# Kernel tuning notes

Hardware: AMD Instinct MI355X
Metric: run time of the kernel (lower is better)

Reference implementation:

```python
import jax, jax.numpy as jnp
import numpy as np

N, E, DIN, DOUT = 50000, 500000, 512, 20
HID = DIN // 4  # 128, from GAT_NET(dim_in, dim_in//4, dim_out)
NEG_SLOPE = 0.2  # PyG GATConv default


def _gat_conv(x, src, dst, Wl, Wr, att_l, att_r, bias, n):
    """PyG GATConv with heads=1: messages flow src -> dst (source_to_target)."""
    xl = x @ Wl.T            # [N, C_out] source-side transform
    xr = x @ Wr.T            # [N, C_out] target-side transform
    el = jnp.sum(xl * att_l, axis=-1)   # [N]
    er = jnp.sum(xr * att_r, axis=-1)   # [N]
    e = jax.nn.leaky_relu(el[src] + er[dst], NEG_SLOPE)  # [E]
    # numerically-stable softmax over incoming edges of each dst node
    emax = jax.ops.segment_max(e, dst, num_segments=n)
    emax = jnp.where(jnp.isfinite(emax), emax, 0.0)  # guard isolated nodes
    w = jnp.exp(e - emax[dst])
    denom = jax.ops.segment_sum(w, dst, num_segments=n)
    alpha = w / (denom[dst] + 1e-16)                     # [E]
    out = jax.ops.segment_sum(xl[src] * alpha[:, None], dst, num_segments=n)
    return out + bias


def setup_inputs() -> dict:
    key = jax.random.key(0)
    ks = jax.random.split(key, 12)
    x = jax.random.normal(ks[0], (N, DIN), dtype=jnp.float32)
    edge_index = jax.random.randint(ks[1], (2, E), 0, N, dtype=jnp.int64)
    # mil_score0: Linear(dim_in, dim_out), init normal(std=0.01), bias 0
    W0 = 0.01 * jax.random.normal(ks[2], (DOUT, DIN), dtype=jnp.float32)
    b0 = jnp.zeros((DOUT,), dtype=jnp.float32)
    # gat1: GATConv(DIN -> HID), gat2: GATConv(HID -> DOUT), glorot-ish scale
    def lin(k, o, i):
        return jax.random.normal(k, (o, i), dtype=jnp.float32) * (1.0 / np.sqrt(i))
    gat1_Wl = lin(ks[3], HID, DIN)
    gat1_Wr = lin(ks[4], HID, DIN)
    gat1_al = jax.random.normal(ks[5], (HID,), dtype=jnp.float32) * 0.1
    gat1_ar = jax.random.normal(ks[6], (HID,), dtype=jnp.float32) * 0.1
    gat1_b = jnp.zeros((HID,), dtype=jnp.float32)
    gat2_Wl = lin(ks[7], DOUT, HID)
    gat2_Wr = lin(ks[8], DOUT, HID)
    gat2_al = jax.random.normal(ks[9], (DOUT,), dtype=jnp.float32) * 0.1
    gat2_ar = jax.random.normal(ks[10], (DOUT,), dtype=jnp.float32) * 0.1
    gat2_b = jnp.zeros((DOUT,), dtype=jnp.float32)
    return {
        "x": x, "edge_index": edge_index, "W0": W0, "b0": b0,
        "gat1_Wl": gat1_Wl, "gat1_Wr": gat1_Wr, "gat1_al": gat1_al,
        "gat1_ar": gat1_ar, "gat1_b": gat1_b,
        "gat2_Wl": gat2_Wl, "gat2_Wr": gat2_Wr, "gat2_al": gat2_al,
        "gat2_ar": gat2_ar, "gat2_b": gat2_b,
    }


def reference(x, edge_index, W0, b0,
              gat1_Wl, gat1_Wr, gat1_al, gat1_ar, gat1_b,
              gat2_Wl, gat2_Wr, gat2_al, gat2_ar, gat2_b):
    n = x.shape[0]
    src, dst = edge_index[0], edge_index[1]
    mil_score0 = x @ W0.T + b0                       # [N, DOUT]
    h = _gat_conv(x, src, dst, gat1_Wl, gat1_Wr, gat1_al, gat1_ar, gat1_b, n)
    h = jax.nn.elu(h)                                # standard GAT inter-layer nonlinearity
    mil_score1 = _gat_conv(h, src, dst, gat2_Wl, gat2_Wr, gat2_al, gat2_ar, gat2_b, n)
    # dual softmax fusion: over proposals (axis=0) * over classes (axis=1)
    return jax.nn.softmax(mil_score0, axis=0) * jax.nn.softmax(mil_score1, axis=1)
```

## Files before the change

### kernel.cpp

```cpp
#include <hip/hip_runtime.h>
#include <math.h>

#define DIN 512
#define HID 128
#define DOUT 20
#define NCAT 160
#define BKP 40
#define NBLK_COL 200
#define SCAN_TILE 1024

typedef unsigned int u32;
typedef unsigned short u16;
using short8 = __attribute__((ext_vector_type(8))) short;
using f32x4  = __attribute__((ext_vector_type(4))) float;

__device__ __forceinline__ u16 f2bf(float f) {
  u32 u = __float_as_uint(f);
  u += 0x7FFFu + ((u >> 16) & 1u);
  return (u16)(u >> 16);
}
__device__ __forceinline__ float bf2f(u16 h) {
  return __uint_as_float(((u32)h) << 16);
}

__global__ void k_prep(const float* __restrict__ W1r, const float* __restrict__ a1r,
                       const float* __restrict__ W2r, const float* __restrict__ a2r,
                       float* __restrict__ vr1, float* __restrict__ vr2) {
  int t = threadIdx.x;
  for (int k = t; k < DIN; k += 256) {
    float s = 0.f;
    for (int c = 0; c < HID; ++c) s = fmaf(a1r[c], W1r[c * DIN + k], s);
    vr1[k] = s;
  }
  if (t < HID) {
    float s = 0.f;
    for (int c = 0; c < DOUT; ++c) s = fmaf(a2r[c], W2r[c * HID + t], s);
    vr2[t] = s;
  }
}

__global__ void k_prepw(const float* __restrict__ W1l, const float* __restrict__ W0,
                        const float* __restrict__ vr1, u16* __restrict__ whcat,
                        u16* __restrict__ wlcat) {
  int idx = blockIdx.x * 256 + threadIdx.x;
  if (idx >= NCAT * DIN) return;
  int c = idx >> 9, k = idx & 511;
  float w = 0.f;
  if (c < HID) w = W1l[c * DIN + k];
  else if (c < HID + DOUT) w = W0[(c - HID) * DIN + k];
  else if (c == HID + DOUT) w = vr1[k];
  u16 h = f2bf(w);
  whcat[idx] = h;
  wlcat[idx] = f2bf(w - bf2f(h));
}

__global__ void k_hist(const int* __restrict__ ei, int* __restrict__ deg, int E) {
  int stride = gridDim.x * blockDim.x;
  for (int e = blockIdx.x * blockDim.x + threadIdx.x; e < E; e += stride)
    atomicAdd(deg + ei[E + e], 1);
}

__launch_bounds__(256)
__global__ void k_scan1(const int* __restrict__ deg, int* __restrict__ tilesum, int M) {
  __shared__ int ws[4];
  int t = threadIdx.x;
  int idx = blockIdx.x * SCAN_TILE + t * 4;
  int4 d = make_int4(0, 0, 0, 0);
  if (idx + 3 < M) d = *(const int4*)(deg + idx);
  else {
    if (idx + 0 < M) d.x = deg[idx + 0];
    if (idx + 1 < M) d.y = deg[idx + 1];
    if (idx + 2 < M) d.z = deg[idx + 2];
    if (idx + 3 < M) d.w = deg[idx + 3];
  }
  int s = d.x + d.y + d.z + d.w;
#pragma unroll
  for (int m = 1; m < 64; m <<= 1) s += __shfl_xor(s, m);
  int lane = t & 63, wave = t >> 6;
  if (lane == 0) ws[wave] = s;
  __syncthreads();
  if (t == 0) tilesum[blockIdx.x] = ws[0] + ws[1] + ws[2] + ws[3];
}

__global__ void k_scan2(const int* __restrict__ tilesum, int* __restrict__ tileoff,
                        int* __restrict__ rowptr, int nb, int M) {
  int t = threadIdx.x;
  int own = (t < nb) ? tilesum[t] : 0;
  int v = own;
#pragma unroll
  for (int off = 1; off < 64; off <<= 1) {
    int u = __shfl_up(v, off);
    if (t >= off) v += u;
  }
  if (t < nb) tileoff[t] = v - own;
  if (t == nb - 1) rowptr[M] = v;
}

__launch_bounds__(256)
__global__ void k_scan3(const int* __restrict__ deg, const int* __restrict__ tileoff,
                        int* __restrict__ rowptr, int* __restrict__ cursor, int M) {
  __shared__ int wsums[4];
  int t = threadIdx.x;
  int idx = blockIdx.x * SCAN_TILE + t * 4;
  int4 d = make_int4(0, 0, 0, 0);
  if (idx + 3 < M) d = *(const int4*)(deg + idx);
  else {
    if (idx + 0 < M) d.x = deg[idx + 0];
    if (idx + 1 < M) d.y = deg[idx + 1];
    if (idx + 2 < M) d.z = deg[idx + 2];
    if (idx + 3 < M) d.w = deg[idx + 3];
  }
  int s0 = d.x, s01 = d.x + d.y, s012 = s01 + d.z, tsum = s012 + d.w;
  int lane = t & 63, wave = t >> 6;
  int v = tsum;
#pragma unroll
  for (int off = 1; off < 64; off <<= 1) {
    int u = __shfl_up(v, off);
    if (lane >= off) v += u;
  }
  if (lane == 63) wsums[wave] = v;
  __syncthreads();
  int woff = 0;
  for (int i = 0; i < wave; ++i) woff += wsums[i];
  int ex = tileoff[blockIdx.x] + woff + (v - tsum);
  if (idx + 0 < M) { rowptr[idx + 0] = ex;        cursor[idx + 0] = ex; }
  if (idx + 1 < M) { rowptr[idx + 1] = ex + s0;   cursor[idx + 1] = ex + s0; }
  if (idx + 2 < M) { rowptr[idx + 2] = ex + s01;  cursor[idx + 2] = ex + s01; }
  if (idx + 3 < M) { rowptr[idx + 3] = ex + s012; cursor[idx + 3] = ex + s012; }
}

__global__ void k_csr(const int* __restrict__ ei, int* __restrict__ cursor,
                      int* __restrict__ csr_src, int E) {
  int stride = gridDim.x * blockDim.x;
  for (int e = blockIdx.x * blockDim.x + threadIdx.x; e < E; e += stride) {
    int d = ei[E + e];
    int p = atomicAdd(cursor + d, 1);
    csr_src[p] = ei[e];
  }
}

__launch_bounds__(256, 4)
__global__ void k_fused1(const float* __restrict__ x, const u16* __restrict__ whcat,
                         const u16* __restrict__ wlcat, const float* __restrict__ b0,
                         float* __restrict__ xl1, float* __restrict__ ms0,
                         float* __restrict__ er1, int M) {
  __shared__ u16 xh_s[64 * BKP];
  __shared__ u16 xl_s[64 * BKP];
  __shared__ u16 wh_s[NCAT * BKP];
  __shared__ u16 wl_s[NCAT * BKP];
  const int tid  = threadIdx.x;
  const int wid  = tid >> 6;
  const int wr   = wid >> 1;
  const int wc   = wid & 1;
  const int lane = tid & 63;
  const int r    = lane & 15;
  const int g    = lane >> 4;
  const int brow = blockIdx.x * 64;

  f32x4 acc[2][5];
#pragma unroll
  for (int mr = 0; mr < 2; ++mr)
#pragma unroll
    for (int nf = 0; nf < 5; ++nf)
      acc[mr][nf] = (f32x4){0.f, 0.f, 0.f, 0.f};

  for (int kt = 0; kt < DIN / 32; ++kt) {
    const int k0 = kt * 32;
    __syncthreads();
#pragma unroll
    for (int i = 0; i < 2; ++i) {
      int s = i * 256 + tid;
      int row = s >> 3, c4 = s & 7;
      int grow = brow + row;
      float4 v = make_float4(0.f, 0.f, 0.f, 0.f);
      if (grow < M) v = *(const float4*)(x + (size_t)grow * DIN + k0 + c4 * 4);
      u16 h0 = f2bf(v.x), h1 = f2bf(v.y), h2 = f2bf(v.z), h3 = f2bf(v.w);
      *(ushort4*)&xh_s[row * BKP + c4 * 4] = make_ushort4(h0, h1, h2, h3);
      *(ushort4*)&xl_s[row * BKP + c4 * 4] =
          make_ushort4(f2bf(v.x - bf2f(h0)), f2bf(v.y - bf2f(h1)),
                       f2bf(v.z - bf2f(h2)), f2bf(v.w - bf2f(h3)));
    }
#pragma unroll
    for (int i = 0; i < 5; ++i) {
      int s = i * 256 + tid;
      int row = s >> 3, c4 = s & 7;
      *(ushort4*)&wh_s[row * BKP + c4 * 4] =
          *(const ushort4*)(whcat + (size_t)row * DIN + k0 + c4 * 4);
      *(ushort4*)&wl_s[row * BKP + c4 * 4] =
          *(const ushort4*)(wlcat + (size_t)row * DIN + k0 + c4 * 4);
    }
    __syncthreads();

    short8 ah[2], alo[2], bh[5], blo[5];
#pragma unroll
    for (int mr = 0; mr < 2; ++mr) {
      int row = wr * 32 + mr * 16 + r;
      ah[mr]  = *(const short8*)&xh_s[row * BKP + g * 8];
      alo[mr] = *(const short8*)&xl_s[row * BKP + g * 8];
    }
#pragma unroll
    for (int nf = 0; nf < 5; ++nf) {
      int col = wc * 80 + nf * 16 + r;
      bh[nf]  = *(const short8*)&wh_s[col * BKP + g * 8];
      blo[nf] = *(const short8*)&wl_s[col * BKP + g * 8];
    }
#pragma unroll
    for (int mr = 0; mr < 2; ++mr)
#pragma unroll
      for (int nf = 0; nf < 5; ++nf) {
        acc[mr][nf] = __builtin_amdgcn_mfma_f32_16x16x32_bf16(ah[mr],  bh[nf],  acc[mr][nf], 0, 0, 0);
        acc[mr][nf] = __builtin_amdgcn_mfma_f32_16x16x32_bf16(ah[mr],  blo[nf], acc[mr][nf], 0, 0, 0);
        acc[mr][nf] = __builtin_amdgcn_mfma_f32_16x16x32_bf16(alo[mr], bh[nf],  acc[mr][nf], 0, 0, 0);
      }
  }

#pragma unroll
  for (int mr = 0; mr < 2; ++mr) {
    int growb = brow + wr * 32 + mr * 16 + g * 4;
#pragma unroll
    for (int nf = 0; nf < 5; ++nf) {
      int gcol = wc * 80 + nf * 16 + r;
#pragma unroll
      for (int q = 0; q < 4; ++q) {
        int grow = growb + q;
        if (grow < M) {
          float v = acc[mr][nf][q];
          if (gcol < HID) xl1[(size_t)grow * HID + gcol] = v;
          else if (gcol < HID + DOUT) ms0[(size_t)grow * DOUT + (gcol - HID)] = v + b0[gcol - HID];
          else if (gcol == HID + DOUT) er1[grow] = v;
        }
      }
    }
  }
}

__launch_bounds__(256)
__global__ void k_el1(const float* __restrict__ xl1, const float* __restrict__ a1l,
                      float* __restrict__ el1, int M) {
  int wv = threadIdx.x >> 6, lane = threadIdx.x & 63;
  int node = blockIdx.x * 4 + wv;
  if (node >= M) return;
  float2 v = *(const float2*)(xl1 + (size_t)node * HID + lane * 2);
  float2 a = *(const float2*)(a1l + lane * 2);
  float s = fmaf(v.y, a.y, v.x * a.x);
#pragma unroll
  for (int m = 1; m < 64; m <<= 1) s += __shfl_xor(s, m);
  if (lane == 0) el1[node] = s;
}

__launch_bounds__(256)
__global__ void k_gath1(const int* __restrict__ rowptr, const int* __restrict__ csr_src,
                        const float* __restrict__ el, const float* __restrict__ er,
                        const float* __restrict__ xl1, float* __restrict__ out1, int M) {
  int g = threadIdx.x >> 6, lane = threadIdx.x & 63;
  int d = blockIdx.x * 4 + g;
  if (d >= M) return;
  int lo = rowptr[d], hi = rowptr[d + 1];
  float erd = er[d];
  float a0 = 0.f, a1 = 0.f, wsum = 0.f;
  for (int j = lo; j < hi; ++j) {
    int s = csr_src[j];
    float v = el[s] + erd;
    v = v >= 0.f ? v : 0.2f * v;
    float w = expf(v);
    wsum += w;
    float2 xv = *(const float2*)(xl1 + (size_t)s * HID + lane * 2);
    a0 = fmaf(w, xv.x, a0);
    a1 = fmaf(w, xv.y, a1);
  }
  float inv = 1.f / (wsum + 1e-16f);
  *(float2*)(out1 + (size_t)d * HID + lane * 2) = make_float2(a0 * inv, a1 * inv);
}

__launch_bounds__(256)
__global__ void k_node2(const float* __restrict__ out1, const float* __restrict__ b1,
                        const float* __restrict__ W2l, const float* __restrict__ a2l,
                        const float* __restrict__ vr2, float* __restrict__ xl2,
                        float* __restrict__ el2, float* __restrict__ er2, int M) {
  int g = threadIdx.x >> 5, lane = threadIdx.x & 31;
  int node = blockIdx.x * 8 + g;
  if (node >= M) return;
  float4 v = *(const float4*)(out1 + (size_t)node * HID + lane * 4);
  float4 bb = *(const float4*)(b1 + lane * 4);
  float h[4] = {v.x + bb.x, v.y + bb.y, v.z + bb.z, v.w + bb.w};
#pragma unroll
  for (int t = 0; t < 4; ++t) h[t] = h[t] > 0.f ? h[t] : expm1f(h[t]);
  float s[21];
#pragma unroll
  for (int j = 0; j < 21; ++j) {
    const float* wr = (j < 20) ? (W2l + (size_t)j * HID) : vr2;
    float4 wv = *(const float4*)(wr + lane * 4);
    float acc;
    acc = fmaf(h[0], wv.x, 0.f);
    acc = fmaf(h[1], wv.y, acc);
    acc = fmaf(h[2], wv.z, acc);
    acc = fmaf(h[3], wv.w, acc);
#pragma unroll
    for (int m = 1; m < 32; m <<= 1) acc += __shfl_xor(acc, m);
    s[j] = acc;
  }
  if (lane == 0) {
    float el = 0.f;
#pragma unroll
    for (int j = 0; j < 20; ++j) {
      xl2[(size_t)node * DOUT + j] = s[j];
      el = fmaf(s[j], a2l[j], el);
    }
    el2[node] = el;
    er2[node] = s[20];
  }
}

__launch_bounds__(256)
__global__ void k_gath2(const int* __restrict__ rowptr, const int* __restrict__ csr_src,
                        const float* __restrict__ el, const float* __restrict__ er,
                        const float* __restrict__ xl2, float* __restrict__ out2, int M) {
  int g = threadIdx.x >> 5, lane = threadIdx.x & 31;
  int d = blockIdx.x * 8 + g;
  if (d >= M) return;
  int lo = rowptr[d], hi = rowptr[d + 1];
  float erd = er[d];
  float acc = 0.f, wsum = 0.f;
  for (int j = lo; j < hi; ++j) {
    int s = csr_src[j];
    float v = el[s] + erd;
    v = v >= 0.f ? v : 0.2f * v;
    float w = expf(v);
    wsum += w;
    if (lane < DOUT) acc = fmaf(w, xl2[(size_t)s * DOUT + lane], acc);
  }
  if (lane < DOUT) out2[(size_t)d * DOUT + lane] = acc / (wsum + 1e-16f);
}

__launch_bounds__(256)
__global__ void k_colsum1(const float* __restrict__ ms0, float* __restrict__ partial, int M) {
  __shared__ float lds[4][20];
  float sm[20];
#pragma unroll
  for (int j = 0; j < 20; ++j) sm[j] = 0.f;
  int stride = gridDim.x * blockDim.x;
  for (int i = blockIdx.x * blockDim.x + threadIdx.x; i < M; i += stride) {
    const float4* row = (const float4*)(ms0 + (size_t)i * DOUT);
#pragma unroll
    for (int q = 0; q < 5; ++q) {
      float4 v = row[q];
      sm[q * 4 + 0] += expf(v.x);
      sm[q * 4 + 1] += expf(v.y);
      sm[q * 4 + 2] += expf(v.z);
      sm[q * 4 + 3] += expf(v.w);
    }
  }
#pragma unroll
  for (int j = 0; j < 20; ++j) {
#pragma unroll
    for (int k = 1; k < 64; k <<= 1) sm[j] += __shfl_xor(sm[j], k);
  }
  int wave = threadIdx.x >> 6, lane = threadIdx.x & 63;
  if (lane == 0) {
#pragma unroll
    for (int j = 0; j < 20; ++j) lds[wave][j] = sm[j];
  }
  __syncthreads();
  if (threadIdx.x < 20)
    partial[blockIdx.x * 20 + threadIdx.x] =
        lds[0][threadIdx.x] + lds[1][threadIdx.x] + lds[2][threadIdx.x] + lds[3][threadIdx.x];
}

__global__ void k_colsum2(const float* __restrict__ partial, float* __restrict__ colsum) {
  int j = threadIdx.x;
  if (j < 20) {
    float s = 0.f;
    for (int b = 0; b < NBLK_COL; ++b) s += partial[b * 20 + j];
    colsum[j] = s;
  }
}

__launch_bounds__(256)
__global__ void k_final(const float* __restrict__ ms0, const float* __restrict__ out2,
                        const float* __restrict__ b2, const float* __restrict__ colsum,
                        float* __restrict__ out, int M) {
  int i = blockIdx.x * 256 + threadIdx.x;
  if (i >= M) return;
  float ms1[20];
  const float4* r2 = (const float4*)(out2 + (size_t)i * DOUT);
#pragma unroll
  for (int q = 0; q < 5; ++q) {
    float4 v = r2[q];
    ms1[q * 4 + 0] = v.x + b2[q * 4 + 0];
    ms1[q * 4 + 1] = v.y + b2[q * 4 + 1];
    ms1[q * 4 + 2] = v.z + b2[q * 4 + 2];
    ms1[q * 4 + 3] = v.w + b2[q * 4 + 3];
  }
  float rmax = -INFINITY;
#pragma unroll
  for (int j = 0; j < 20; ++j) rmax = fmaxf(rmax, ms1[j]);
  float rsum = 0.f;
#pragma unroll
  for (int j = 0; j < 20; ++j) { ms1[j] = expf(ms1[j] - rmax); rsum += ms1[j]; }
  const float4* r0 = (const float4*)(ms0 + (size_t)i * DOUT);
  float o[20];
#pragma unroll
  for (int q = 0; q < 5; ++q) {
    float4 v = r0[q];
    o[q * 4 + 0] = expf(v.x) / colsum[q * 4 + 0] * (ms1[q * 4 + 0] / rsum);
    o[q * 4 + 1] = expf(v.y) / colsum[q * 4 + 1] * (ms1[q * 4 + 1] / rsum);
    o[q * 4 + 2] = expf(v.z) / colsum[q * 4 + 2] * (ms1[q * 4 + 2] / rsum);
    o[q * 4 + 3] = expf(v.w) / colsum[q * 4 + 3] * (ms1[q * 4 + 3] / rsum);
  }
  float4* po = (float4*)(out + (size_t)i * DOUT);
#pragma unroll
  for (int q = 0; q < 5; ++q)
    po[q] = make_float4(o[q * 4 + 0], o[q * 4 + 1], o[q * 4 + 2], o[q * 4 + 3]);
}

extern "C" void kernel_launch(void* const* d_in, const int* in_sizes, int n_in,
                              void* d_out, int out_size, void* d_ws, size_t ws_size,
                              hipStream_t stream) {
  const float* x   = (const float*)d_in[0];
  const int*   ei  = (const int*)d_in[1];
  const float* W0  = (const float*)d_in[2];
  const float* b0  = (const float*)d_in[3];
  const float* W1l = (const float*)d_in[4];
  const float* W1r = (const float*)d_in[5];
  const float* a1l = (const float*)d_in[6];
  const float* a1r = (const float*)d_in[7];
  const float* b1  = (const float*)d_in[8];
  const float* W2l = (const float*)d_in[9];
  const float* W2r = (const float*)d_in[10];
  const float* a2l = (const float*)d_in[11];
  const float* a2r = (const float*)d_in[12];
  const float* b2  = (const float*)d_in[13];
  const int M = in_sizes[0] / DIN;
  const int E = in_sizes[1] / 2;
  const int NB_SCAN = (M + SCAN_TILE - 1) / SCAN_TILE;
  (void)n_in; (void)out_size; (void)ws_size;

  char* w = (char*)d_ws;
  size_t off = 0;
  auto alloc = [&](size_t bytes) -> void* {
    void* p = w + off;
    off += (bytes + 255) & ~(size_t)255;
    return p;
  };
  float* xl1     = (float*)alloc((size_t)M * HID * 4);
  float* el1     = (float*)alloc((size_t)M * 4);
  float* er1     = (float*)alloc((size_t)M * 4);
  float* ms0     = (float*)alloc((size_t)M * DOUT * 4);
  float* out1    = (float*)alloc((size_t)M * HID * 4);
  float* xl2     = (float*)alloc((size_t)M * DOUT * 4);
  float* el2     = (float*)alloc((size_t)M * 4);
  float* er2     = (float*)alloc((size_t)M * 4);
  float* out2    = (float*)alloc((size_t)M * DOUT * 4);
  float* partial = (float*)alloc((size_t)NBLK_COL * 20 * 4);
  float* colsum  = (float*)alloc(32 * 4);
  float* vr1     = (float*)alloc(DIN * 4);
  float* vr2     = (float*)alloc(HID * 4);
  u16*   whcat   = (u16*)alloc((size_t)NCAT * DIN * 2);
  u16*   wlcat   = (u16*)alloc((size_t)NCAT * DIN * 2);
  int*   deg     = (int*)alloc((size_t)M * 4);
  int*   rowptr  = (int*)alloc((size_t)(M + 1) * 4);
  int*   cursor  = (int*)alloc((size_t)M * 4);
  int*   csr_src = (int*)alloc((size_t)E * 4);
  int*   tilesum = (int*)alloc(64 * 4);
  int*   tileoff = (int*)alloc(64 * 4);

  hipMemsetAsync(deg, 0, (size_t)M * 4, stream);

  k_prep<<<1, 256, 0, stream>>>(W1r, a1r, W2r, a2r, vr1, vr2);
  k_prepw<<<(NCAT * DIN + 255) / 256, 256, 0, stream>>>(W1l, W0, vr1, whcat, wlcat);
  k_hist<<<1024, 256, 0, stream>>>(ei, deg, E);
  k_scan1<<<NB_SCAN, 256, 0, stream>>>(deg, tilesum, M);
  k_scan2<<<1, 64, 0, stream>>>(tilesum, tileoff, rowptr, NB_SCAN, M);
  k_scan3<<<NB_SCAN, 256, 0, stream>>>(deg, tileoff, rowptr, cursor, M);
  k_csr<<<1024, 256, 0, stream>>>(ei, cursor, csr_src, E);

  k_fused1<<<(M + 63) / 64, 256, 0, stream>>>(x, whcat, wlcat, b0, xl1, ms0, er1, M);
  k_el1<<<(M + 3) / 4, 256, 0, stream>>>(xl1, a1l, el1, M);

  k_gath1<<<(M + 3) / 4, 256, 0, stream>>>(rowptr, csr_src, el1, er1, xl1, out1, M);
  k_node2<<<(M + 7) / 8, 256, 0, stream>>>(out1, b1, W2l, a2l, vr2, xl2, el2, er2, M);
  k_gath2<<<(M + 7) / 8, 256, 0, stream>>>(rowptr, csr_src, el2, er2, xl2, out2, M);

  k_colsum1<<<NBLK_COL, 256, 0, stream>>>(ms0, partial, M);
  k_colsum2<<<1, 64, 0, stream>>>(partial, colsum);
  k_final<<<(M + 255) / 256, 256, 0, stream>>>(ms0, out2, b2, colsum, (float*)d_out, M);
}
```

Before: 438.9 us.

## Pre-swizzle weights into MFMA fragment layout and fuse el1 into GEMM

The weight matrices are now pre-arranged by k_prepw into a per-lane MFMA fragment layout, so each wave loads B fragments straight from global/L2 instead of staging them through LDS. Each wave now owns 16 rows and all 160 columns, and the launch bound drops to 2 blocks per CU. The el1 attention dot product is computed from the accumulators in the GEMM epilogue, which removes the separate k_el1 kernel and its re-read of xl1. This trades LDS traffic and one launch for repeated global weight loads per wave and higher register pressure.

```diff
diff --git a/kernel.cpp b/kernel.cpp
--- a/kernel.cpp
+++ b/kernel.cpp
@@ -8,6 +8,7 @@
 #define BKP 40
 #define NBLK_COL 200
 #define SCAN_TILE 1024
+#define NFRAG (10 * 16 * 64 * 8)
 
 typedef unsigned int u32;
 typedef unsigned short u16;
@@ -40,18 +41,20 @@
 }
 
 __global__ void k_prepw(const float* __restrict__ W1l, const float* __restrict__ W0,
-                        const float* __restrict__ vr1, u16* __restrict__ whcat,
-                        u16* __restrict__ wlcat) {
+                        const float* __restrict__ vr1, u16* __restrict__ whf,
+                        u16* __restrict__ wlf) {
   int idx = blockIdx.x * 256 + threadIdx.x;
-  if (idx >= NCAT * DIN) return;
-  int c = idx >> 9, k = idx & 511;
+  if (idx >= NFRAG) return;
+  int j = idx & 7, lane = (idx >> 3) & 63, kt = (idx >> 9) & 15, ct = idx >> 13;
+  int col = ct * 16 + (lane & 15);
+  int k = kt * 32 + (lane >> 4) * 8 + j;
   float w = 0.f;
-  if (c < HID) w = W1l[c * DIN + k];
-  else if (c < HID + DOUT) w = W0[(c - HID) * DIN + k];
-  else if (c == HID + DOUT) w = vr1[k];
+  if (col < HID) w = W1l[col * DIN + k];
+  else if (col < HID + DOUT) w = W0[(col - HID) * DIN + k];
+  else if (col == HID + DOUT) w = vr1[k];
   u16 h = f2bf(w);
-  whcat[idx] = h;
-  wlcat[idx] = f2bf(w - bf2f(h));
+  whf[idx] = h;
+  wlf[idx] = f2bf(w - bf2f(h));
 }
 
 __global__ void k_hist(const int* __restrict__ ei, int* __restrict__ deg, int E) {
@@ -139,32 +142,26 @@
   }
 }
 
-__launch_bounds__(256, 4)
-__global__ void k_fused1(const float* __restrict__ x, const u16* __restrict__ whcat,
-                         const u16* __restrict__ wlcat, const float* __restrict__ b0,
+__launch_bounds__(256, 2)
+__global__ void k_fused1(const float* __restrict__ x, const u16* __restrict__ whf,
+                         const u16* __restrict__ wlf, const float* __restrict__ b0,
+                         const float* __restrict__ a1l,
                          float* __restrict__ xl1, float* __restrict__ ms0,
-                         float* __restrict__ er1, int M) {
+                         float* __restrict__ er1, float* __restrict__ el1, int M) {
   __shared__ u16 xh_s[64 * BKP];
   __shared__ u16 xl_s[64 * BKP];
-  __shared__ u16 wh_s[NCAT * BKP];
-  __shared__ u16 wl_s[NCAT * BKP];
   const int tid  = threadIdx.x;
   const int wid  = tid >> 6;
-  const int wr   = wid >> 1;
-  const int wc   = wid & 1;
   const int lane = tid & 63;
   const int r    = lane & 15;
   const int g    = lane >> 4;
   const int brow = blockIdx.x * 64;
 
-  f32x4 acc[2][5];
-#pragma unroll
-  for (int mr = 0; mr < 2; ++mr)
-#pragma unroll
-    for (int nf = 0; nf < 5; ++nf)
-      acc[mr][nf] = (f32x4){0.f, 0.f, 0.f, 0.f};
-
-  for (int kt = 0; kt < DIN / 32; ++kt) {
+  f32x4 acc[10];
+#pragma unroll
+  for (int ct = 0; ct < 10; ++ct) acc[ct] = (f32x4){0.f, 0.f, 0.f, 0.f};
+
+  for (int kt = 0; kt < 16; ++kt) {
     const int k0 = kt * 32;
     __syncthreads();
 #pragma unroll
@@ -180,72 +177,60 @@
           make_ushort4(f2bf(v.x - bf2f(h0)), f2bf(v.y - bf2f(h1)),
                        f2bf(v.z - bf2f(h2)), f2bf(v.w - bf2f(h3)));
     }
-#pragma unroll
-    for (int i = 0; i < 5; ++i) {
-      int s = i * 256 + tid;
-      int row = s >> 3, c4 = s & 7;
-      *(ushort4*)&wh_s[row * BKP + c4 * 4] =
-          *(const ushort4*)(whcat + (size_t)row * DIN + k0 + c4 * 4);
-      *(ushort4*)&wl_s[row * BKP + c4 * 4] =
-          *(const ushort4*)(wlcat + (size_t)row * DIN + k0 + c4 * 4);
+    __syncthreads();
+
+    const int arow = wid * 16 + r;
+    short8 ah  = *(const short8*)&xh_s[arow * BKP + g * 8];
+    short8 alo = *(const short8*)&xl_s[arow * BKP + g * 8];
+
+#pragma unroll
+    for (int ct = 0; ct < 10; ++ct) {
+      const size_t fb = (((size_t)ct * 16 + kt) * 64 + lane) * 8;
+      short8 bh  = *(const short8*)(whf + fb);
+      short8 blo = *(const short8*)(wlf + fb);
+      acc[ct] = __builtin_amdgcn_mfma_f32_16x16x32_bf16(ah,  bh,  acc[ct], 0, 0, 0);
+      acc[ct] = __builtin_amdgcn_mfma_f32_16x16x32_bf16(ah,  blo, acc[ct], 0, 0, 0);
+      acc[ct] = __builtin_amdgcn_mfma_f32_16x16x32_bf16(alo, bh,  acc[ct], 0, 0, 0);
     }
-    __syncthreads();
-
-    short8 ah[2], alo[2], bh[5], blo[5];
-#pragma unroll
-    for (int mr = 0; mr < 2; ++mr) {
-      int row = wr * 32 + mr * 16 + r;
-      ah[mr]  = *(const short8*)&xh_s[row * BKP + g * 8];
-      alo[mr] = *(const short8*)&xl_s[row * BKP + g * 8];
-    }
-#pragma unroll
-    for (int nf = 0; nf < 5; ++nf) {
-      int col = wc * 80 + nf * 16 + r;
-      bh[nf]  = *(const short8*)&wh_s[col * BKP + g * 8];
-      blo[nf] = *(const short8*)&wl_s[col * BKP + g * 8];
-    }
-#pragma unroll
-    for (int mr = 0; mr < 2; ++mr)
-#pragma unroll
-      for (int nf = 0; nf < 5; ++nf) {
-        acc[mr][nf] = __builtin_amdgcn_mfma_f32_16x16x32_bf16(ah[mr],  bh[nf],  acc[mr][nf], 0, 0, 0);
-        acc[mr][nf] = __builtin_amdgcn_mfma_f32_16x16x32_bf16(ah[mr],  blo[nf], acc[mr][nf], 0, 0, 0);
-        acc[mr][nf] = __builtin_amdgcn_mfma_f32_16x16x32_bf16(alo[mr], bh[nf],  acc[mr][nf], 0, 0, 0);
-      }
-  }
-
-#pragma unroll
-  for (int mr = 0; mr < 2; ++mr) {
-    int growb = brow + wr * 32 + mr * 16 + g * 4;
-#pragma unroll
-    for (int nf = 0; nf < 5; ++nf) {
-      int gcol = wc * 80 + nf * 16 + r;
-#pragma unroll
-      for (int q = 0; q < 4; ++q) {
-        int grow = growb + q;
-        if (grow < M) {
-          float v = acc[mr][nf][q];
-          if (gcol < HID) xl1[(size_t)grow * HID + gcol] = v;
-          else if (gcol < HID + DOUT) ms0[(size_t)grow * DOUT + (gcol - HID)] = v + b0[gcol - HID];
-          else if (gcol == HID + DOUT) er1[grow] = v;
-        }
+  }
+
+  const int growb = brow + wid * 16 + g * 4;
+#pragma unroll
+  for (int ct = 0; ct < 10; ++ct) {
+    int gcol = ct * 16 + r;
+#pragma unroll
+    for (int q = 0; q < 4; ++q) {
+      int grow = growb + q;
+      if (grow < M) {
+        float v = acc[ct][q];
+        if (gcol < HID) xl1[(size_t)grow * HID + gcol] = v;
+        else if (gcol < HID + DOUT) ms0[(size_t)grow * DOUT + (gcol - HID)] = v + b0[gcol - HID];
+        else if (gcol == HID + DOUT) er1[grow] = v;
       }
     }
   }
-}
-
-__launch_bounds__(256)
-__global__ void k_el1(const float* __restrict__ xl1, const float* __restrict__ a1l,
-                      float* __restrict__ el1, int M) {
-  int wv = threadIdx.x >> 6, lane = threadIdx.x & 63;
-  int node = blockIdx.x * 4 + wv;
-  if (node >= M) return;
-  float2 v = *(const float2*)(xl1 + (size_t)node * HID + lane * 2);
-  float2 a = *(const float2*)(a1l + lane * 2);
-  float s = fmaf(v.y, a.y, v.x * a.x);
-#pragma unroll
-  for (int m = 1; m < 64; m <<= 1) s += __shfl_xor(s, m);
-  if (lane == 0) el1[node] = s;
+  float part0 = 0.f, part1 = 0.f, part2 = 0.f, part3 = 0.f;
+#pragma unroll
+  for (int ct = 0; ct < 8; ++ct) {
+    float a = a1l[ct * 16 + r];
+    part0 = fmaf(acc[ct][0], a, part0);
+    part1 = fmaf(acc[ct][1], a, part1);
+    part2 = fmaf(acc[ct][2], a, part2);
+    part3 = fmaf(acc[ct][3], a, part3);
+  }
+#pragma unroll
+  for (int m = 1; m < 16; m <<= 1) {
+    part0 += __shfl_xor(part0, m);
+    part1 += __shfl_xor(part1, m);
+    part2 += __shfl_xor(part2, m);
+    part3 += __shfl_xor(part3, m);
+  }
+  if (r == 0) {
+    if (growb + 0 < M) el1[growb + 0] = part0;
+    if (growb + 1 < M) el1[growb + 1] = part1;
+    if (growb + 2 < M) el1[growb + 2] = part2;
+    if (growb + 3 < M) el1[growb + 3] = part3;
+  }
 }
 
 __launch_bounds__(256)
@@ -455,8 +440,8 @@
   float* colsum  = (float*)alloc(32 * 4);
   float* vr1     = (float*)alloc(DIN * 4);
   float* vr2     = (float*)alloc(HID * 4);
-  u16*   whcat   = (u16*)alloc((size_t)NCAT * DIN * 2);
-  u16*   wlcat   = (u16*)alloc((size_t)NCAT * DIN * 2);
+  u16*   whf     = (u16*)alloc((size_t)NFRAG * 2);
+  u16*   wlf     = (u16*)alloc((size_t)NFRAG * 2);
   int*   deg     = (int*)alloc((size_t)M * 4);
   int*   rowptr  = (int*)alloc((size_t)(M + 1) * 4);
   int*   cursor  = (int*)alloc((size_t)M * 4);
@@ -467,15 +452,15 @@
   hipMemsetAsync(deg, 0, (size_t)M * 4, stream);
 
   k_prep<<<1, 256, 0, stream>>>(W1r, a1r, W2r, a2r, vr1, vr2);
-  k_prepw<<<(NCAT * DIN + 255) / 256, 256, 0, stream>>>(W1l, W0, vr1, whcat, wlcat);
+  k_prepw<<<(NFRAG + 255) / 256, 256, 0, stream>>>(W1l, W0, vr1, whf, wlf);
   k_hist<<<1024, 256, 0, stream>>>(ei, deg, E);
   k_scan1<<<NB_SCAN, 256, 0, stream>>>(deg, tilesum, M);
   k_scan2<<<1, 64, 0, stream>>>(tilesum, tileoff, rowptr, NB_SCAN, M);
   k_scan3<<<NB_SCAN, 256, 0, stream>>>(deg, tileoff, rowptr, cursor, M);
   k_csr<<<1024, 256, 0, stream>>>(ei, cursor, csr_src, E);
 
-  k_fused1<<<(M + 63) / 64, 256, 0, stream>>>(x, whcat, wlcat, b0, xl1, ms0, er1, M);
-  k_el1<<<(M + 3) / 4, 256, 0, stream>>>(xl1, a1l, el1, M);
+  k_fused1<<<(M + 63) / 64, 256, 0, stream>>>(x, whf, wlf, b0, a1l,
+                                              xl1, ms0, er1, el1, M);
 
   k_gath1<<<(M + 3) / 4, 256, 0, stream>>>(rowptr, csr_src, el1, er1, xl1, out1, M);
   k_node2<<<(M + 7) / 8, 256, 0, stream>>>(out1, b1, W2l, a2l, vr2, xl2, el2, er2, M);
```

Result: slower. 478.0 us (+8.9%).
